# Kernel optimization log

Hardware: AMD Instinct MI355X
Metric: run time of the kernel (lower is better)

The kernel has to match this reference:

```python
import jax, jax.numpy as jnp
import numpy as np

B, S, D, H = 4, 2048, 2048, 8192  # batch, seq, d_model, hidden (power of 2 for FHT)


def fwht(x):
    """Fast Walsh-Hadamard transform along the last axis, normalized by 1/sqrt(n).

    Iterative butterfly: O(n log n). n must be a power of 2.
    """
    orig_shape = x.shape
    n = orig_shape[-1]
    x = x.reshape(-1, n)
    h = 1
    while h < n:
        # view as (rows, n/(2h) blocks, 2 halves, h) and do the butterfly
        xb = x.reshape(-1, n // (2 * h), 2, h)
        a = xb[:, :, 0, :]
        b = xb[:, :, 1, :]
        x = jnp.stack([a + b, a - b], axis=2).reshape(-1, n)
        h *= 2
    scale = jnp.asarray(1.0 / np.sqrt(n), dtype=x.dtype)
    return (x * scale).reshape(orig_shape)


def setup_inputs() -> dict:
    key = jax.random.key(0)
    kx, k1, k2, k3 = jax.random.split(key, 4)
    x = jax.random.normal(kx, (B, S, D), dtype=jnp.float32)
    # nn.Linear weights: [out_features, in_features], no bias (Llama FFN style)
    W1 = jax.random.normal(k1, (H, D), dtype=jnp.float32) * (1.0 / np.sqrt(D))
    W2 = jax.random.normal(k2, (D, H), dtype=jnp.float32) * (1.0 / np.sqrt(H))
    W3 = jax.random.normal(k3, (H, D), dtype=jnp.float32) * (1.0 / np.sqrt(D))
    return {"x": x, "W1": W1, "W2": W2, "W3": W3}


def reference(x, W1, W2, W3):
    # w2( fht( silu(w1(x)) * w3(x) ) )
    up_gate = jnp.einsum("bsd,hd->bsh", x, W1)          # w1(x): [B,S,H]
    up_lin = jnp.einsum("bsd,hd->bsh", x, W3)           # w3(x): [B,S,H]
    hidden = jax.nn.silu(up_gate) * up_lin              # SwiGLU gate
    hidden = fwht(hidden)                               # fast Hadamard transform over H
    out = jnp.einsum("bsh,dh->bsd", hidden, W2)         # w2(.): [B,S,D]
    return out
```

## Files before the change

### kernel.cpp

```cpp
#include <hip/hip_runtime.h>

typedef __attribute__((ext_vector_type(8))) __bf16 bf16x8;
typedef __attribute__((ext_vector_type(4))) float f32x4;

#define GLOAD_LDS16(g, l)                                                     \
  __builtin_amdgcn_global_load_lds(                                           \
      (const __attribute__((address_space(1))) void*)(g),                     \
      (__attribute__((address_space(3))) void*)(l), 16, 0, 0)

#define BAR() __builtin_amdgcn_s_barrier()
#define SB0() __builtin_amdgcn_sched_barrier(0)
#define LGKM(n)                                                               \
  do {                                                                        \
    asm volatile("s_waitcnt lgkmcnt(" #n ")" ::: "memory");                   \
    SB0();                                                                    \
  } while (0)
#define VMCNT0() asm volatile("s_waitcnt vmcnt(0)" ::: "memory")
#define PRIO1() __builtin_amdgcn_s_setprio(1)
#define PRIO0() __builtin_amdgcn_s_setprio(0)
#define MFMA_BF16 __builtin_amdgcn_mfma_f32_16x16x32_bf16

__device__ __forceinline__ unsigned short f32_to_bf16(float f) {
  unsigned int u = __builtin_bit_cast(unsigned int, f);
  u += 0x7FFFu + ((u >> 16) & 1u);
  return (unsigned short)(u >> 16);
}

__global__ void conv_f32_bf16(const float* __restrict__ in,
                              unsigned short* __restrict__ out, int n4) {
  int stride = gridDim.x * blockDim.x;
  for (int i = blockIdx.x * blockDim.x + threadIdx.x; i < n4; i += stride) {
    float4 v = reinterpret_cast<const float4*>(in)[i];
    ushort4 o;
    o.x = f32_to_bf16(v.x);
    o.y = f32_to_bf16(v.y);
    o.z = f32_to_bf16(v.z);
    o.w = f32_to_bf16(v.w);
    reinterpret_cast<ushort4*>(out)[i] = o;
  }
}

__global__ void fwht_rows_bf16(const float* __restrict__ in,
                               unsigned short* __restrict__ out) {
  __shared__ float s[8192];
  const int tid = threadIdx.x;
  const float* row = in + (size_t)blockIdx.x * 8192;
#pragma unroll
  for (int i = 0; i < 8; ++i)
    reinterpret_cast<float4*>(s)[tid + i * 256] =
        reinterpret_cast<const float4*>(row)[tid + i * 256];
  for (int h = 1; h < 8192; h <<= 1) {
    __syncthreads();
#pragma unroll
    for (int it = 0; it < 16; ++it) {
      int i = tid + it * 256;
      int j = ((i & ~(h - 1)) << 1) | (i & (h - 1));
      float a = s[j], b = s[j + h];
      s[j] = a + b;
      s[j + h] = a - b;
    }
  }
  __syncthreads();
  const float scale = 0.011048543456039806f;
  unsigned short* orow = out + (size_t)blockIdx.x * 8192;
#pragma unroll
  for (int i = 0; i < 8; ++i) {
    float4 v = reinterpret_cast<const float4*>(s)[tid + i * 256];
    ushort4 o;
    o.x = f32_to_bf16(v.x * scale);
    o.y = f32_to_bf16(v.y * scale);
    o.z = f32_to_bf16(v.z * scale);
    o.w = f32_to_bf16(v.w * scale);
    reinterpret_cast<ushort4*>(orow)[tid + i * 256] = o;
  }
}

#define G2_TILE(BI, tt)                                                       \
  {                                                                           \
    if ((tt) + 1 < NT) {                                                      \
      unsigned short* dA = L + (((BI) ^ 1) * 16384) + wid * 512;              \
      unsigned short* dB = L + 32768 + (((BI) ^ 1) * 16384) + wid * 512;      \
      _Pragma("unroll") for (int i = 0; i < 4; ++i) {                         \
        GLOAD_LDS16(pA + i * s64, dA + i * 4096);                             \
        GLOAD_LDS16(pB + i * s64, dB + i * 4096);                             \
      }                                                                       \
    }                                                                         \
    SB0();                                                                    \
    _Pragma("unroll") for (int m = 0; m < 4; ++m) {                           \
      ra[m][0] = *(const bf16x8*)(Lb + ((BI)*32768 + m * 2048) + rA0);        \
      ra[m][1] = *(const bf16x8*)(Lb + ((BI)*32768 + m * 2048) + rA1);        \
    }                                                                         \
    _Pragma("unroll") for (int n = 0; n < 2; ++n) {                           \
      rb[n][0] = *(const bf16x8*)(Lb + ((BI)*32768 + n * 2048) + rB0);        \
      rb[n][1] = *(const bf16x8*)(Lb + ((BI)*32768 + n * 2048) + rB1);        \
    }                                                                         \
    SB0();                                                                    \
    _Pragma("unroll") for (int n = 2; n < 4; ++n) {                           \
      rb[n][0] = *(const bf16x8*)(Lb + ((BI)*32768 + n * 2048) + rB0);        \
      rb[n][1] = *(const bf16x8*)(Lb + ((BI)*32768 + n * 2048) + rB1);        \
    }                                                                         \
    SB0();                                                                    \
    LGKM(4);                                                                  \
    PRIO1();                                                                  \
    _Pragma("unroll") for (int m = 0; m < 4; ++m)                             \
        _Pragma("unroll") for (int n = 0; n < 2; ++n) {                       \
      acc[m][n] = MFMA_BF16(ra[m][0], rb[n][0], acc[m][n], 0, 0, 0);          \
      acc[m][n] = MFMA_BF16(ra[m][1], rb[n][1], acc[m][n], 0, 0, 0);          \
    }                                                                         \
    PRIO0();                                                                  \
    SB0();                                                                    \
    LGKM(0);                                                                  \
    PRIO1();                                                                  \
    _Pragma("unroll") for (int m = 0; m < 4; ++m)                             \
        _Pragma("unroll") for (int n = 2; n < 4; ++n) {                       \
      acc[m][n] = MFMA_BF16(ra[m][0], rb[n][0], acc[m][n], 0, 0, 0);          \
      acc[m][n] = MFMA_BF16(ra[m][1], rb[n][1], acc[m][n], 0, 0, 0);          \
    }                                                                         \
    PRIO0();                                                                  \
    SB0();                                                                    \
    _Pragma("unroll") for (int m = 0; m < 4; ++m) {                           \
      ra[m][0] = *(const bf16x8*)(Lb + ((BI)*32768 + (m + 4) * 2048) + rA0);  \
      ra[m][1] = *(const bf16x8*)(Lb + ((BI)*32768 + (m + 4) * 2048) + rA1);  \
    }                                                                         \
    SB0();                                                                    \
    LGKM(0);                                                                  \
    PRIO1();                                                                  \
    _Pragma("unroll") for (int m = 0; m < 4; ++m)                             \
        _Pragma("unroll") for (int n = 2; n < 4; ++n) {                       \
      acc[4 + m][n] = MFMA_BF16(ra[m][0], rb[n][0], acc[4 + m][n], 0, 0, 0);  \
      acc[4 + m][n] = MFMA_BF16(ra[m][1], rb[n][1], acc[4 + m][n], 0, 0, 0);  \
    }                                                                         \
    _Pragma("unroll") for (int m = 0; m < 4; ++m)                             \
        _Pragma("unroll") for (int n = 0; n < 2; ++n) {                       \
      acc[4 + m][n] = MFMA_BF16(ra[m][0], rb[n][0], acc[4 + m][n], 0, 0, 0);  \
      acc[4 + m][n] = MFMA_BF16(ra[m][1], rb[n][1], acc[4 + m][n], 0, 0, 0);  \
    }                                                                         \
    PRIO0();                                                                  \
    VMCNT0();                                                                 \
    BAR();                                                                    \
    pA += 128;                                                                \
    pB += 128;                                                                \
  }

__launch_bounds__(512, 2)
__global__ void gemm2_pipe(const unsigned short* __restrict__ A,
                           const unsigned short* __restrict__ Bt,
                           float* __restrict__ C, int M, int N, int K) {
  __shared__ __align__(16) unsigned short L[65536];
  const int tid = threadIdx.x, lane = tid & 63, wid = tid >> 6;
  const int wr = wid >> 2, wc = wid & 3;
  const int nbx = N >> 8;
  const int cpx = (int)gridDim.x >> 3;
  const int swz = ((int)blockIdx.x & 7) * cpx + ((int)blockIdx.x >> 3);
  const int bm = (swz / nbx) << 8, bn = (swz % nbx) << 8;
  const int NT = K >> 6;

  const int lp0 = (lane & 15) * 128 + (((lane >> 4) << 4) ^ ((lane & 7) << 4));
  const int lp1 =
      (lane & 15) * 128 + ((64 | ((lane >> 4) << 4)) ^ ((lane & 7) << 4));
  const int rA0 = wr * 16384 + lp0, rA1 = wr * 16384 + lp1;
  const int rB0 = 65536 + wc * 8192 + lp0, rB1 = 65536 + wc * 8192 + lp1;

  const int swzc = ((lane & 7) ^ (lane >> 3)) << 4;
  const char* pA = (const char*)A +
                   ((size_t)(bm + (wid << 3) + (lane >> 3)) * K) * 2 + swzc;
  const char* pB = (const char*)Bt +
                   ((size_t)(bn + (wid << 3) + (lane >> 3)) * K) * 2 + swzc;
  const size_t s64 = (size_t)K * 128;
  const char* Lb = (const char*)L;

  {
    unsigned short* dA = L + wid * 512;
    unsigned short* dB = L + 32768 + wid * 512;
#pragma unroll
    for (int i = 0; i < 4; ++i) {
      GLOAD_LDS16(pA + i * s64, dA + i * 4096);
      GLOAD_LDS16(pB + i * s64, dB + i * 4096);
    }
  }
  pA += 128;
  pB += 128;

  f32x4 acc[8][4];
#pragma unroll
  for (int m = 0; m < 8; ++m)
#pragma unroll
    for (int n = 0; n < 4; ++n) acc[m][n] = (f32x4)0.0f;
  bf16x8 ra[4][2], rb[4][2];

  VMCNT0();
  BAR();

  for (int t = 0; t < NT; t += 2) {
    G2_TILE(0, t)
    G2_TILE(1, t + 1)
  }

  const int er = (lane >> 4) << 2;
  const int ec = lane & 15;
#pragma unroll
  for (int mi = 0; mi < 8; ++mi)
#pragma unroll
    for (int n = 0; n < 4; ++n)
#pragma unroll
      for (int r = 0; r < 4; ++r) {
        size_t row = (size_t)(bm + wr * 128 + mi * 16 + er + r);
        size_t col = (size_t)(bn + wc * 64 + n * 16 + ec);
        C[row * N + col] = acc[mi][n][r];
      }
}

#define G1_TILE(BI, tt)                                                       \
  {                                                                           \
    if ((tt) + 1 < NT) {                                                      \
      unsigned short* dA = L + (((BI) ^ 1) * 16384) + wid * 512;              \
      unsigned short* dB1 = L + 32768 + (((BI) ^ 1) * 8192) + wid * 512;      \
      unsigned short* dB3 = L + 49152 + (((BI) ^ 1) * 8192) + wid * 512;      \
      _Pragma("unroll") for (int i = 0; i < 4; ++i)                           \
          GLOAD_LDS16(pA + i * s64, dA + i * 4096);                           \
      _Pragma("unroll") for (int i = 0; i < 2; ++i) {                         \
        GLOAD_LDS16(pB1 + i * s64, dB1 + i * 4096);                           \
        GLOAD_LDS16(pB3 + i * s64, dB3 + i * 4096);                           \
      }                                                                       \
    }                                                                         \
    SB0();                                                                    \
    _Pragma("unroll") for (int m = 0; m < 4; ++m) {                           \
      ra[m][0] = *(const bf16x8*)(Lb + ((BI)*32768 + m * 2048) + rA0);        \
      ra[m][1] = *(const bf16x8*)(Lb + ((BI)*32768 + m * 2048) + rA1);        \
    }                                                                         \
    _Pragma("unroll") for (int n = 0; n < 2; ++n) {                           \
      rb[n][0] = *(const bf16x8*)(Lb + ((BI)*16384 + n * 2048) + rB0);        \
      rb[n][1] = *(const bf16x8*)(Lb + ((BI)*16384 + n * 2048) + rB1);        \
    }                                                                         \
    SB0();                                                                    \
    _Pragma("unroll") for (int n = 2; n < 4; ++n) {                           \
      rb[n][0] = *(const bf16x8*)(Lb + ((BI)*16384 + n * 2048) + rB0);        \
      rb[n][1] = *(const bf16x8*)(Lb + ((BI)*16384 + n * 2048) + rB1);        \
    }                                                                         \
    SB0();                                                                    \
    LGKM(4);                                                                  \
    PRIO1();                                                                  \
    _Pragma("unroll") for (int m = 0; m < 4; ++m)                             \
        _Pragma("unroll") for (int n = 0; n < 2; ++n) {                       \
      accG[m][n] = MFMA_BF16(ra[m][0], rb[n][0], accG[m][n], 0, 0, 0);        \
      accG[m][n] = MFMA_BF16(ra[m][1], rb[n][1], accG[m][n], 0, 0, 0);        \
    }                                                                         \
    PRIO0();                                                                  \
    SB0();                                                                    \
    LGKM(0);                                                                  \
    PRIO1();                                                                  \
    _Pragma("unroll") for (int m = 0; m < 4; ++m)                             \
        _Pragma("unroll") for (int n = 2; n < 4; ++n) {                       \
      accG[m][n] = MFMA_BF16(ra[m][0], rb[n][0], accG[m][n], 0, 0, 0);        \
      accG[m][n] = MFMA_BF16(ra[m][1], rb[n][1], accG[m][n], 0, 0, 0);        \
    }                                                                         \
    PRIO0();                                                                  \
    SB0();                                                                    \
    _Pragma("unroll") for (int n = 2; n < 4; ++n) {        \
      rb[n][0] = *(const bf16x8*)(Lb + (32768 + (BI)*16384 + n * 2048) + rB0);\
      rb[n][1] = *(const bf16x8*)(Lb + (32768 + (BI)*16384 + n * 2048) + rB1);\
    }                                                                         \
    SB0();                                                                    \
    _Pragma("unroll") for (int n = 0; n < 2; ++n) {                           \
      rb[n][0] = *(const bf16x8*)(Lb + (32768 + (BI)*16384 + n * 2048) + rB0);\
      rb[n][1] = *(const bf16x8*)(Lb + (32768 + (BI)*16384 + n * 2048) + rB1);\
    }                                                                         \
    SB0();                                                                    \
    LGKM(4);                                                                  \
    PRIO1();                                                                  \
    _Pragma("unroll") for (int m = 0; m < 4; ++m)                             \
        _Pragma("unroll") for (int n = 2; n < 4; ++n) {                       \
      accL[m][n] = MFMA_BF16(ra[m][0], rb[n][0], accL[m][n], 0, 0, 0);        \
      accL[m][n] = MFMA_BF16(ra[m][1], rb[n][1], accL[m][n], 0, 0, 0);        \
    }                                                                         \
    PRIO0();                                                                  \
    SB0();                                                                    \
    LGKM(0);                                                                  \
    PRIO1();                                                                  \
    _Pragma("unroll") for (int m = 0; m < 4; ++m)                             \
        _Pragma("unroll") for (int n = 0; n < 2; ++n) {                       \
      accL[m][n] = MFMA_BF16(ra[m][0], rb[n][0], accL[m][n], 0, 0, 0);        \
      accL[m][n] = MFMA_BF16(ra[m][1], rb[n][1], accL[m][n], 0, 0, 0);        \
    }                                                                         \
    PRIO0();                                                                  \
    VMCNT0();                                                                 \
    BAR();                                                                    \
    pA += 128;                                                                \
    pB1 += 128;                                                               \
    pB3 += 128;                                                               \
  }

__launch_bounds__(512, 2)
__global__ void gemm1_pipe(const unsigned short* __restrict__ A,
                           const unsigned short* __restrict__ B1p,
                           const unsigned short* __restrict__ B3p,
                           unsigned short* __restrict__ Hout, int M, int N,
                           int K) {
  __shared__ __align__(16) unsigned short L[65536];
  const int tid = threadIdx.x, lane = tid & 63, wid = tid >> 6;
  const int wr = wid >> 1, wc = wid & 1;
  const int nby = M >> 8;
  const int cpx = (int)gridDim.x >> 3;
  const int swz = ((int)blockIdx.x & 7) * cpx + ((int)blockIdx.x >> 3);
  const int bm = (swz % nby) << 8;
  const int bn = (swz / nby) << 7;
  const int NT = K >> 6;

  const int lp0 = (lane & 15) * 128 + (((lane >> 4) << 4) ^ ((lane & 7) << 4));
  const int lp1 =
      (lane & 15) * 128 + ((64 | ((lane >> 4) << 4)) ^ ((lane & 7) << 4));
  const int rA0 = wr * 8192 + lp0, rA1 = wr * 8192 + lp1;
  const int rB0 = 65536 + wc * 8192 + lp0, rB1 = 65536 + wc * 8192 + lp1;

  const int swzc = ((lane & 7) ^ (lane >> 3)) << 4;
  const char* pA = (const char*)A +
                   ((size_t)(bm + (wid << 3) + (lane >> 3)) * K) * 2 + swzc;
  const char* pB1 = (const char*)B1p +
                    ((size_t)(bn + (wid << 3) + (lane >> 3)) * K) * 2 + swzc;
  const char* pB3 = (const char*)B3p +
                    ((size_t)(bn + (wid << 3) + (lane >> 3)) * K) * 2 + swzc;
  const size_t s64 = (size_t)K * 128;
  const char* Lb = (const char*)L;

  {
    unsigned short* dA = L + wid * 512;
    unsigned short* dB1 = L + 32768 + wid * 512;
    unsigned short* dB3 = L + 49152 + wid * 512;
#pragma unroll
    for (int i = 0; i < 4; ++i) GLOAD_LDS16(pA + i * s64, dA + i * 4096);
#pragma unroll
    for (int i = 0; i < 2; ++i) {
      GLOAD_LDS16(pB1 + i * s64, dB1 + i * 4096);
      GLOAD_LDS16(pB3 + i * s64, dB3 + i * 4096);
    }
  }
  pA += 128;
  pB1 += 128;
  pB3 += 128;

  f32x4 accG[4][4], accL[4][4];
#pragma unroll
  for (int m = 0; m < 4; ++m)
#pragma unroll
    for (int n = 0; n < 4; ++n) {
      accG[m][n] = (f32x4)0.0f;
      accL[m][n] = (f32x4)0.0f;
    }
  bf16x8 ra[4][2], rb[4][2];

  VMCNT0();
  BAR();

  for (int t = 0; t < NT; t += 2) {
    G1_TILE(0, t)
    G1_TILE(1, t + 1)
  }

  const int er = (lane >> 4) << 2;
  const int ec = lane & 15;
#pragma unroll
  for (int m = 0; m < 4; ++m)
#pragma unroll
    for (int n = 0; n < 4; ++n)
#pragma unroll
      for (int r = 0; r < 4; ++r) {
        float g = accG[m][n][r];
        float li = accL[m][n][r];
        float h = (g / (1.0f + __expf(-g))) * li;
        size_t row = (size_t)(bm + wr * 64 + m * 16 + er + r);
        size_t col = (size_t)(bn + wc * 64 + n * 16 + ec);
        Hout[row * N + col] = f32_to_bf16(h);
      }
}

extern "C" void kernel_launch(void* const* d_in, const int* in_sizes, int n_in,
                              void* d_out, int out_size, void* d_ws,
                              size_t ws_size, hipStream_t stream) {
  const float* x = (const float*)d_in[0];
  const float* W1 = (const float*)d_in[1];
  const float* W2 = (const float*)d_in[2];
  const float* W3 = (const float*)d_in[3];
  float* out = (float*)d_out;

  const int M = 8192, D = 2048, H = 8192;
  const size_t NE = (size_t)16777216;

  unsigned short* xb = (unsigned short*)d_ws;
  unsigned short* w1b = xb + NE;
  unsigned short* w3b = w1b + NE;
  unsigned short* w2f = w3b + NE;
  unsigned short* hid = w2f + NE;

  conv_f32_bf16<<<2048, 256, 0, stream>>>(x, xb, (int)(NE / 4));
  conv_f32_bf16<<<2048, 256, 0, stream>>>(W1, w1b, (int)(NE / 4));
  conv_f32_bf16<<<2048, 256, 0, stream>>>(W3, w3b, (int)(NE / 4));
  fwht_rows_bf16<<<2048, 256, 0, stream>>>(W2, w2f);

  gemm1_pipe<<<(M / 256) * (H / 128), 512, 0, stream>>>(xb, w1b, w3b, hid, M,
                                                        H, D);
  gemm2_pipe<<<(M / 256) * (D / 256), 512, 0, stream>>>(hid, w2f, out, M, D,
                                                        H);
}
```

Baseline: 811.5 us.

## Interleave LDS fragment reads with MFMA sub-blocks in both GEMM tiles

Splits each K-tile of the two GEMM kernels into finer phases. Each phase issues the LDS reads for the next sub-block of A or B fragments while MFMAs run on already-loaded fragments. It waits with lgkmcnt(4) instead of draining all LDS reads. Separate register buffers are added (ra2 in gemm2, rb1/rb3 in gemm1) so the next reads do not overwrite fragments still in use. The aim is to hide LDS read latency behind matrix-core work, at the cost of higher VGPR pressure under the 512-thread, 2-block launch bounds, which could cause spills.

```diff
diff --git a/kernel.cpp b/kernel.cpp
--- a/kernel.cpp
+++ b/kernel.cpp
@@ -75,66 +75,78 @@
   }
 }
 
-#define G2_TILE(BI, tt)                                                       \
+#define RD_A(arr, mi, bi)                                                     \
+  arr[0] = *(const bf16x8*)(Lb + ((bi)*32768 + (mi)*2048) + rA0);             \
+  arr[1] = *(const bf16x8*)(Lb + ((bi)*32768 + (mi)*2048) + rA1);
+#define RD_B(arr, ni, bi)                                                     \
+  arr[0] = *(const bf16x8*)(Lb + ((bi)*32768 + (ni)*2048) + rB0);             \
+  arr[1] = *(const bf16x8*)(Lb + ((bi)*32768 + (ni)*2048) + rB1);
+
+#define G2_TILE(bi, tt)                                                       \
   {                                                                           \
     if ((tt) + 1 < NT) {                                                      \
-      unsigned short* dA = L + (((BI) ^ 1) * 16384) + wid * 512;              \
-      unsigned short* dB = L + 32768 + (((BI) ^ 1) * 16384) + wid * 512;      \
+      unsigned short* dA = L + (((bi) ^ 1) * 16384) + wid * 512;              \
+      unsigned short* dB = L + 32768 + (((bi) ^ 1) * 16384) + wid * 512;      \
       _Pragma("unroll") for (int i = 0; i < 4; ++i) {                         \
         GLOAD_LDS16(pA + i * s64, dA + i * 4096);                             \
         GLOAD_LDS16(pB + i * s64, dB + i * 4096);                             \
       }                                                                       \
     }                                                                         \
     SB0();                                                                    \
-    _Pragma("unroll") for (int m = 0; m < 4; ++m) {                           \
-      ra[m][0] = *(const bf16x8*)(Lb + ((BI)*32768 + m * 2048) + rA0);        \
-      ra[m][1] = *(const bf16x8*)(Lb + ((BI)*32768 + m * 2048) + rA1);        \
-    }                                                                         \
-    _Pragma("unroll") for (int n = 0; n < 2; ++n) {                           \
-      rb[n][0] = *(const bf16x8*)(Lb + ((BI)*32768 + n * 2048) + rB0);        \
-      rb[n][1] = *(const bf16x8*)(Lb + ((BI)*32768 + n * 2048) + rB1);        \
-    }                                                                         \
-    SB0();                                                                    \
-    _Pragma("unroll") for (int n = 2; n < 4; ++n) {                           \
-      rb[n][0] = *(const bf16x8*)(Lb + ((BI)*32768 + n * 2048) + rB0);        \
-      rb[n][1] = *(const bf16x8*)(Lb + ((BI)*32768 + n * 2048) + rB1);        \
-    }                                                                         \
-    SB0();                                                                    \
-    LGKM(4);                                                                  \
-    PRIO1();                                                                  \
-    _Pragma("unroll") for (int m = 0; m < 4; ++m)                             \
-        _Pragma("unroll") for (int n = 0; n < 2; ++n) {                       \
-      acc[m][n] = MFMA_BF16(ra[m][0], rb[n][0], acc[m][n], 0, 0, 0);          \
-      acc[m][n] = MFMA_BF16(ra[m][1], rb[n][1], acc[m][n], 0, 0, 0);          \
-    }                                                                         \
+                                       \
+    RD_A(ra[0], 0, bi) RD_A(ra[1], 1, bi)                                     \
+    RD_B(rb[0], 0, bi) RD_B(rb[1], 1, bi)                                     \
+    SB0();                                                                    \
+                                                        \
+    RD_A(ra[2], 2, bi) RD_A(ra[3], 3, bi)                                     \
+    SB0();                                                                    \
+    LGKM(4);                                                                  \
+    PRIO1();                                                                  \
+    _Pragma("unroll") for (int ks = 0; ks < 2; ++ks)                          \
+        _Pragma("unroll") for (int m = 0; m < 2; ++m)                         \
+            _Pragma("unroll") for (int n = 0; n < 2; ++n) acc[m][n] =         \
+                MFMA_BF16(ra[m][ks], rb[n][ks], acc[m][n], 0, 0, 0);          \
+    PRIO0();                                                                  \
+    SB0();                                                                    \
+                                                        \
+    RD_B(rb[2], 2, bi) RD_B(rb[3], 3, bi)                                     \
+    SB0();                                                                    \
+    LGKM(4);                                                                  \
+    PRIO1();                                                                  \
+    _Pragma("unroll") for (int ks = 0; ks < 2; ++ks)                          \
+        _Pragma("unroll") for (int m = 2; m < 4; ++m)                         \
+            _Pragma("unroll") for (int n = 0; n < 2; ++n) acc[m][n] =         \
+                MFMA_BF16(ra[m][ks], rb[n][ks], acc[m][n], 0, 0, 0);          \
+    PRIO0();                                                                  \
+    SB0();                                                                    \
+                                                       \
+    RD_A(ra2[0], 4, bi) RD_A(ra2[1], 5, bi)                                   \
+    SB0();                                                                    \
+    LGKM(4);                                                                  \
+    PRIO1();                                                                  \
+    _Pragma("unroll") for (int ks = 0; ks < 2; ++ks)                          \
+        _Pragma("unroll") for (int m = 0; m < 4; ++m)                         \
+            _Pragma("unroll") for (int n = 2; n < 4; ++n) acc[m][n] =         \
+                MFMA_BF16(ra[m][ks], rb[n][ks], acc[m][n], 0, 0, 0);          \
+    PRIO0();                                                                  \
+    SB0();                                                                    \
+                                                       \
+    RD_A(ra2[2], 6, bi) RD_A(ra2[3], 7, bi)                                   \
+    SB0();                                                                    \
+    LGKM(4);                                                                  \
+    PRIO1();                                                                  \
+    _Pragma("unroll") for (int ks = 0; ks < 2; ++ks)                          \
+        _Pragma("unroll") for (int m = 0; m < 2; ++m)                         \
+            _Pragma("unroll") for (int n = 0; n < 4; ++n) acc[4 + m][n] =     \
+                MFMA_BF16(ra2[m][ks], rb[n][ks], acc[4 + m][n], 0, 0, 0);     \
     PRIO0();                                                                  \
     SB0();                                                                    \
     LGKM(0);                                                                  \
     PRIO1();                                                                  \
-    _Pragma("unroll") for (int m = 0; m < 4; ++m)                             \
-        _Pragma("unroll") for (int n = 2; n < 4; ++n) {                       \
-      acc[m][n] = MFMA_BF16(ra[m][0], rb[n][0], acc[m][n], 0, 0, 0);          \
-      acc[m][n] = MFMA_BF16(ra[m][1], rb[n][1], acc[m][n], 0, 0, 0);          \
-    }                                                                         \
-    PRIO0();                                                                  \
-    SB0();                                                                    \
-    _Pragma("unroll") for (int m = 0; m < 4; ++m) {                           \
-      ra[m][0] = *(const bf16x8*)(Lb + ((BI)*32768 + (m + 4) * 2048) + rA0);  \
-      ra[m][1] = *(const bf16x8*)(Lb + ((BI)*32768 + (m + 4) * 2048) + rA1);  \
-    }                                                                         \
-    SB0();                                                                    \
-    LGKM(0);                                                                  \
-    PRIO1();                                                                  \
-    _Pragma("unroll") for (int m = 0; m < 4; ++m)                             \
-        _Pragma("unroll") for (int n = 2; n < 4; ++n) {                       \
-      acc[4 + m][n] = MFMA_BF16(ra[m][0], rb[n][0], acc[4 + m][n], 0, 0, 0);  \
-      acc[4 + m][n] = MFMA_BF16(ra[m][1], rb[n][1], acc[4 + m][n], 0, 0, 0);  \
-    }                                                                         \
-    _Pragma("unroll") for (int m = 0; m < 4; ++m)                             \
-        _Pragma("unroll") for (int n = 0; n < 2; ++n) {                       \
-      acc[4 + m][n] = MFMA_BF16(ra[m][0], rb[n][0], acc[4 + m][n], 0, 0, 0);  \
-      acc[4 + m][n] = MFMA_BF16(ra[m][1], rb[n][1], acc[4 + m][n], 0, 0, 0);  \
-    }                                                                         \
+    _Pragma("unroll") for (int ks = 0; ks < 2; ++ks)                          \
+        _Pragma("unroll") for (int m = 2; m < 4; ++m)                         \
+            _Pragma("unroll") for (int n = 0; n < 4; ++n) acc[4 + m][n] =     \
+                MFMA_BF16(ra2[m][ks], rb[n][ks], acc[4 + m][n], 0, 0, 0);     \
     PRIO0();                                                                  \
     VMCNT0();                                                                 \
     BAR();                                                                    \
@@ -186,7 +198,7 @@
   for (int m = 0; m < 8; ++m)
 #pragma unroll
     for (int n = 0; n < 4; ++n) acc[m][n] = (f32x4)0.0f;
-  bf16x8 ra[4][2], rb[4][2];
+  bf16x8 ra[4][2], ra2[4][2], rb[4][2];
 
   VMCNT0();
   BAR();
@@ -210,12 +222,22 @@
       }
 }
 
-#define G1_TILE(BI, tt)                                                       \
+#define RD_A1(arr, mi, bi)                                                    \
+  arr[0] = *(const bf16x8*)(Lb + ((bi)*32768 + (mi)*2048) + rA0);             \
+  arr[1] = *(const bf16x8*)(Lb + ((bi)*32768 + (mi)*2048) + rA1);
+#define RD_B1(arr, ni, bi)                                                    \
+  arr[0] = *(const bf16x8*)(Lb + (65536 + (bi)*16384 + (ni)*2048) + rBp0);    \
+  arr[1] = *(const bf16x8*)(Lb + (65536 + (bi)*16384 + (ni)*2048) + rBp1);
+#define RD_B3(arr, ni, bi)                                                    \
+  arr[0] = *(const bf16x8*)(Lb + (98304 + (bi)*16384 + (ni)*2048) + rBp0);    \
+  arr[1] = *(const bf16x8*)(Lb + (98304 + (bi)*16384 + (ni)*2048) + rBp1);
+
+#define G1_TILE(bi, tt)                                                       \
   {                                                                           \
     if ((tt) + 1 < NT) {                                                      \
-      unsigned short* dA = L + (((BI) ^ 1) * 16384) + wid * 512;              \
-      unsigned short* dB1 = L + 32768 + (((BI) ^ 1) * 8192) + wid * 512;      \
-      unsigned short* dB3 = L + 49152 + (((BI) ^ 1) * 8192) + wid * 512;      \
+      unsigned short* dA = L + (((bi) ^ 1) * 16384) + wid * 512;              \
+      unsigned short* dB1 = L + 32768 + (((bi) ^ 1) * 8192) + wid * 512;      \
+      unsigned short* dB3 = L + 49152 + (((bi) ^ 1) * 8192) + wid * 512;      \
       _Pragma("unroll") for (int i = 0; i < 4; ++i)                           \
           GLOAD_LDS16(pA + i * s64, dA + i * 4096);                           \
       _Pragma("unroll") for (int i = 0; i < 2; ++i) {                         \
@@ -224,64 +246,60 @@
       }                                                                       \
     }                                                                         \
     SB0();                                                                    \
-    _Pragma("unroll") for (int m = 0; m < 4; ++m) {                           \
-      ra[m][0] = *(const bf16x8*)(Lb + ((BI)*32768 + m * 2048) + rA0);        \
-      ra[m][1] = *(const bf16x8*)(Lb + ((BI)*32768 + m * 2048) + rA1);        \
-    }                                                                         \
-    _Pragma("unroll") for (int n = 0; n < 2; ++n) {                           \
-      rb[n][0] = *(const bf16x8*)(Lb + ((BI)*16384 + n * 2048) + rB0);        \
-      rb[n][1] = *(const bf16x8*)(Lb + ((BI)*16384 + n * 2048) + rB1);        \
-    }                                                                         \
-    SB0();                                                                    \
-    _Pragma("unroll") for (int n = 2; n < 4; ++n) {                           \
-      rb[n][0] = *(const bf16x8*)(Lb + ((BI)*16384 + n * 2048) + rB0);        \
-      rb[n][1] = *(const bf16x8*)(Lb + ((BI)*16384 + n * 2048) + rB1);        \
-    }                                                                         \
-    SB0();                                                                    \
-    LGKM(4);                                                                  \
-    PRIO1();                                                                  \
-    _Pragma("unroll") for (int m = 0; m < 4; ++m)                             \
-        _Pragma("unroll") for (int n = 0; n < 2; ++n) {                       \
-      accG[m][n] = MFMA_BF16(ra[m][0], rb[n][0], accG[m][n], 0, 0, 0);        \
-      accG[m][n] = MFMA_BF16(ra[m][1], rb[n][1], accG[m][n], 0, 0, 0);        \
-    }                                                                         \
+                                      \
+    RD_A1(ra[0], 0, bi) RD_A1(ra[1], 1, bi)                                   \
+    RD_B1(rb1[0], 0, bi) RD_B1(rb1[1], 1, bi)                                 \
+    SB0();                                                                    \
+                                                        \
+    RD_A1(ra[2], 2, bi) RD_A1(ra[3], 3, bi)                                   \
+    SB0();                                                                    \
+    LGKM(4);                                                                  \
+    PRIO1();                                                                  \
+    _Pragma("unroll") for (int ks = 0; ks < 2; ++ks)                          \
+        _Pragma("unroll") for (int m = 0; m < 2; ++m)                         \
+            _Pragma("unroll") for (int n = 0; n < 2; ++n) accG[m][n] =        \
+                MFMA_BF16(ra[m][ks], rb1[n][ks], accG[m][n], 0, 0, 0);        \
+    PRIO0();                                                                  \
+    SB0();                                                                    \
+                                                       \
+    RD_B1(rb1[2], 2, bi) RD_B1(rb1[3], 3, bi)                                 \
+    SB0();                                                                    \
+    LGKM(4);                                                                  \
+    PRIO1();                                                                  \
+    _Pragma("unroll") for (int ks = 0; ks < 2; ++ks)                          \
+        _Pragma("unroll") for (int m = 2; m < 4; ++m)                         \
+            _Pragma("unroll") for (int n = 0; n < 2; ++n) accG[m][n] =        \
+                MFMA_BF16(ra[m][ks], rb1[n][ks], accG[m][n], 0, 0, 0);        \
+    PRIO0();                                                                  \
+    SB0();                                                                    \
+                                                       \
+    RD_B3(rb3[2], 2, bi) RD_B3(rb3[3], 3, bi)                                 \
+    SB0();                                                                    \
+    LGKM(4);                                                                  \
+    PRIO1();                                                                  \
+    _Pragma("unroll") for (int ks = 0; ks < 2; ++ks)                          \
+        _Pragma("unroll") for (int m = 0; m < 4; ++m)                         \
+            _Pragma("unroll") for (int n = 2; n < 4; ++n) accG[m][n] =        \
+                MFMA_BF16(ra[m][ks], rb1[n][ks], accG[m][n], 0, 0, 0);        \
+    PRIO0();                                                                  \
+    SB0();                                                                    \
+                                                       \
+    RD_B3(rb3[0], 0, bi) RD_B3(rb3[1], 1, bi)                                 \
+    SB0();                                                                    \
+    LGKM(4);                                                                  \
+    PRIO1();                                                                  \
+    _Pragma("unroll") for (int ks = 0; ks < 2; ++ks)                          \
+        _Pragma("unroll") for (int m = 0; m < 4; ++m)                         \
+            _Pragma("unroll") for (int n = 2; n < 4; ++n) accL[m][n] =        \
+                MFMA_BF16(ra[m][ks], rb3[n][ks], accL[m][n], 0, 0, 0);        \
     PRIO0();                                                                  \
     SB0();                                                                    \
     LGKM(0);                                                                  \
     PRIO1();                                                                  \
-    _Pragma("unroll") for (int m = 0; m < 4; ++m)                             \
-        _Pragma("unroll") for (int n = 2; n < 4; ++n) {                       \
-      accG[m][n] = MFMA_BF16(ra[m][0], rb[n][0], accG[m][n], 0, 0, 0);        \
-      accG[m][n] = MFMA_BF16(ra[m][1], rb[n][1], accG[m][n], 0, 0, 0);        \
-    }                                                                         \
-    PRIO0();                                                                  \
-    SB0();                                                                    \
-    _Pragma("unroll") for (int n = 2; n < 4; ++n) {        \
-      rb[n][0] = *(const bf16x8*)(Lb + (32768 + (BI)*16384 + n * 2048) + rB0);\
-      rb[n][1] = *(const bf16x8*)(Lb + (32768 + (BI)*16384 + n * 2048) + rB1);\
-    }                                                                         \
-    SB0();                                                                    \
-    _Pragma("unroll") for (int n = 0; n < 2; ++n) {                           \
-      rb[n][0] = *(const bf16x8*)(Lb + (32768 + (BI)*16384 + n * 2048) + rB0);\
-      rb[n][1] = *(const bf16x8*)(Lb + (32768 + (BI)*16384 + n * 2048) + rB1);\
-    }                                                                         \
-    SB0();                                                                    \
-    LGKM(4);                                                                  \
-    PRIO1();                                                                  \
-    _Pragma("unroll") for (int m = 0; m < 4; ++m)                             \
-        _Pragma("unroll") for (int n = 2; n < 4; ++n) {                       \
-      accL[m][n] = MFMA_BF16(ra[m][0], rb[n][0], accL[m][n], 0, 0, 0);        \
-      accL[m][n] = MFMA_BF16(ra[m][1], rb[n][1], accL[m][n], 0, 0, 0);        \
-    }                                                                         \
-    PRIO0();                                                                  \
-    SB0();                                                                    \
-    LGKM(0);                                                                  \
-    PRIO1();                                                                  \
-    _Pragma("unroll") for (int m = 0; m < 4; ++m)                             \
-        _Pragma("unroll") for (int n = 0; n < 2; ++n) {                       \
-      accL[m][n] = MFMA_BF16(ra[m][0], rb[n][0], accL[m][n], 0, 0, 0);        \
-      accL[m][n] = MFMA_BF16(ra[m][1], rb[n][1], accL[m][n], 0, 0, 0);        \
-    }                                                                         \
+    _Pragma("unroll") for (int ks = 0; ks < 2; ++ks)                          \
+        _Pragma("unroll") for (int m = 0; m < 4; ++m)                         \
+            _Pragma("unroll") for (int n = 0; n < 2; ++n) accL[m][n] =        \
+                MFMA_BF16(ra[m][ks], rb3[n][ks], accL[m][n], 0, 0, 0);        \
     PRIO0();                                                                  \
     VMCNT0();                                                                 \
     BAR();                                                                    \
@@ -310,7 +328,7 @@
   const int lp1 =
       (lane & 15) * 128 + ((64 | ((lane >> 4) << 4)) ^ ((lane & 7) << 4));
   const int rA0 = wr * 8192 + lp0, rA1 = wr * 8192 + lp1;
-  const int rB0 = 65536 + wc * 8192 + lp0, rB1 = 65536 + wc * 8192 + lp1;
+  const int rBp0 = wc * 8192 + lp0, rBp1 = wc * 8192 + lp1;
 
   const int swzc = ((lane & 7) ^ (lane >> 3)) << 4;
   const char* pA = (const char*)A +
@@ -346,7 +364,7 @@
       accG[m][n] = (f32x4)0.0f;
       accL[m][n] = (f32x4)0.0f;
     }
-  bf16x8 ra[4][2], rb[4][2];
+  bf16x8 ra[4][2], rb1[4][2], rb3[4][2];
 
   VMCNT0();
   BAR();
```

Measured after the change: 812.7 us. No clear change (+0.2%).
